# Performance work log

Measured on AMD Instinct MI355X. Metric: run time of the kernel, lower is better.

The kernel has to match this reference:

```python
import jax, jax.numpy as jnp
import numpy as np

N = 50000      # nodes
E = 800000     # edges (before self-loops)
IN = 256       # in_channels
OUT = 64       # out_channels per head
H = 4          # heads (layer 0)
LEAKY = 0.2    # PyG GATConv negative_slope default


def setup_inputs() -> dict:
    key = jax.random.key(0)
    ks = jax.random.split(key, 16)
    g = 0.1
    inp = {
        "x": jax.random.normal(ks[0], (N, IN), jnp.float32),
        "edge_index": jax.random.randint(ks[1], (2, E), 0, N, dtype=jnp.int32),
        # layer 0: in -> H*OUT, concat=True
        "W0": jax.random.normal(ks[2], (IN, H * OUT), jnp.float32) * g,
        "a_src0": jax.random.normal(ks[3], (H, OUT), jnp.float32) * g,
        "a_dst0": jax.random.normal(ks[4], (H, OUT), jnp.float32) * g,
        "b0": jnp.zeros((H * OUT,), jnp.float32),
        # layer 1: H*OUT -> OUT, heads=1, concat=False
        "W1": jax.random.normal(ks[5], (H * OUT, OUT), jnp.float32) * g,
        "a_src1": jax.random.normal(ks[6], (1, OUT), jnp.float32) * g,
        "a_dst1": jax.random.normal(ks[7], (1, OUT), jnp.float32) * g,
        "b1": jnp.zeros((OUT,), jnp.float32),
        # layer 2: H*OUT -> OUT (input is OUT from layer 1? no: layer1 outputs OUT)
        "W2": jax.random.normal(ks[8], (OUT, OUT), jnp.float32) * g,
        "a_src2": jax.random.normal(ks[9], (1, OUT), jnp.float32) * g,
        "a_dst2": jax.random.normal(ks[10], (1, OUT), jnp.float32) * g,
        "b2": jnp.zeros((OUT,), jnp.float32),
    }
    return inp


def _gat_layer(x, src, dst, W, a_s, a_d, b, heads, concat):
    """PyG GATConv: per-head linear, edge attention logits, segment softmax
    over incoming edges of each destination node, scatter-sum aggregate."""
    n = x.shape[0]
    h = (x @ W).reshape(n, heads, -1)                      # [N, H, C]
    al_s = (h * a_s).sum(-1)                               # [N, H]
    al_d = (h * a_d).sum(-1)                               # [N, H]
    e = jax.nn.leaky_relu(al_s[src] + al_d[dst], LEAKY)    # [E', H]
    m = jax.ops.segment_max(e, dst, num_segments=n)        # [N, H]
    ex = jnp.exp(e - m[dst])
    den = jax.ops.segment_sum(ex, dst, num_segments=n)     # [N, H]
    alpha = ex / (den[dst] + 1e-16)                        # [E', H]
    out = jax.ops.segment_sum(alpha[:, :, None] * h[src], dst, num_segments=n)  # [N,H,C]
    out = out.reshape(n, -1) if concat else out.mean(axis=1)
    return out + b


def reference(x, edge_index, W0, a_src0, a_dst0, b0, W1, a_src1, a_dst1, b1,
              W2, a_src2, a_dst2, b2):
    n = x.shape[0]
    loop = jnp.arange(n, dtype=edge_index.dtype)
    src = jnp.concatenate([edge_index[0], loop])   # PyG add_self_loops=True
    dst = jnp.concatenate([edge_index[1], loop])
    h = _gat_layer(x, src, dst, W0, a_src0, a_dst0, b0, H, True)
    h = jax.nn.elu(h)
    h = _gat_layer(h, src, dst, W1, a_src1, a_dst1, b1, 1, False)
    h = jax.nn.elu(h)
    h = _gat_layer(h, src, dst, W2, a_src2, a_dst2, b2, 1, False)
    h = jax.nn.elu(h)
    return h
```

## Files before the change

### kernel.cpp

```cpp
#include <hip/hip_runtime.h>
#include <hip/hip_bf16.h>


typedef unsigned short ushort_t;
typedef __attribute__((ext_vector_type(8))) short short8;
typedef __attribute__((ext_vector_type(4))) float f32x4;

__device__ __forceinline__ float elu_f(float x){ return x > 0.f ? x : expm1f(x); }
__device__ __forceinline__ float lrelu_f(float x){ return x > 0.f ? x : 0.2f * x; }
__device__ __forceinline__ ushort_t f2b(float f){
  union { float f; unsigned u; } v; v.f = f;
  unsigned r = v.u + 0x7fff + ((v.u >> 16) & 1);
  return (ushort_t)(r >> 16);
}
__device__ __forceinline__ float b2f_lo(unsigned v){
  union { unsigned u; float f; } c; c.u = v << 16; return c.f;
}
__device__ __forceinline__ float b2f_hi(unsigned v){
  union { unsigned u; float f; } c; c.u = v & 0xffff0000u; return c.f;
}

__global__ __launch_bounds__(256) void prep_kernel(const int* __restrict__ ei,
                                                   int* __restrict__ cnt,
                                                   const float4* __restrict__ x4,
                                                   ushort4* __restrict__ xb4, int n4,
                                                   const float* __restrict__ W0,
                                                   ushort_t* __restrict__ W0p,
                                                   const float* __restrict__ W1,
                                                   ushort_t* __restrict__ W1p,
                                                   const float* __restrict__ W2,
                                                   ushort_t* __restrict__ W2p,
                                                   int E, int Etot, int eb, int fb){
  int bid = blockIdx.x; int t = threadIdx.x;
  if(bid < eb){
    int e = bid * 256 + t;
    if(e < Etot){
      int d = (e < E) ? ei[E + e] : (e - E);
      atomicAdd(&cnt[d], 1);
    }
  } else if(bid < eb + fb){
    int i = (bid - eb) * 256 + t;
    if(i < n4){
      float4 v = x4[i];
      ushort4 o;
      o.x = f2b(v.x); o.y = f2b(v.y); o.z = f2b(v.z); o.w = f2b(v.w);
      xb4[i] = o;
    }
  } else {
    int r = bid - eb - fb;
    if(r < 256){
      int i = r * 256 + t; int k = i >> 8, n = i & 255;
      W0p[(size_t)n * 256 + k] = f2b(W0[i]);
    } else if(r < 320){
      int i = (r - 256) * 256 + t; int k = i >> 6, n = i & 63;
      W1p[(size_t)n * 256 + k] = f2b(W1[i]);
    } else {
      int i = (r - 320) * 256 + t; int k = i >> 6, n = i & 63;
      W2p[(size_t)n * 64 + k] = f2b(W2[i]);
    }
  }
}

__global__ __launch_bounds__(256) void blocksum_kernel(const int* __restrict__ cnt,
                                                       int* __restrict__ bsum, int N){
  __shared__ int sm[256];
  int t = threadIdx.x;
  int i = blockIdx.x * 256 + t;
  sm[t] = (i < N) ? cnt[i] : 0;
  __syncthreads();
  for(int off = 128; off > 0; off >>= 1){
    if(t < off) sm[t] += sm[t + off];
    __syncthreads();
  }
  if(t == 0) bsum[blockIdx.x] = sm[0];
}

__global__ __launch_bounds__(256) void scan2_kernel(const int* __restrict__ cnt,
                                                    const int* __restrict__ bsum,
                                                    int* __restrict__ rowptr,
                                                    int* __restrict__ cursor,
                                                    int N, int Etot, int nb){
  __shared__ int sm[256];
  __shared__ int spfx;
  int t = threadIdx.x;
  int c = blockIdx.x;
  sm[t] = (t < c && t < nb) ? bsum[t] : 0;
  __syncthreads();
  for(int off = 128; off > 0; off >>= 1){
    if(t < off) sm[t] += sm[t + off];
    __syncthreads();
  }
  if(t == 0) spfx = sm[0];
  __syncthreads();
  int pfx = spfx;
  __syncthreads();
  int i = c * 256 + t;
  int v = (i < N) ? cnt[i] : 0;
  sm[t] = v;
  __syncthreads();
  for(int off = 1; off < 256; off <<= 1){
    int x = 0;
    if(t >= off) x = sm[t - off];
    __syncthreads();
    sm[t] += x;
    __syncthreads();
  }
  if(i < N){
    int ex = sm[t] - v + pfx;
    rowptr[i] = ex;
    cursor[i] = ex;
    if(i == N - 1) rowptr[N] = Etot;
  }
}

__global__ __launch_bounds__(256) void scatter_kernel(const int* __restrict__ ei,
                                                      int* __restrict__ cursor,
                                                      int* __restrict__ esrc,
                                                      int E, int Etot){
  int e = blockIdx.x * 256 + threadIdx.x;
  if(e >= Etot) return;
  int s, d;
  if(e < E){ s = ei[e]; d = ei[E + e]; } else { s = e - E; d = s; }
  int pos = atomicAdd(&cursor[d], 1);
  esrc[pos] = s;
}

#define SKP 264
__global__ __launch_bounds__(256) void gemm0_kernel(const ushort_t* __restrict__ A,
                                                    const ushort_t* __restrict__ Bp,
                                                    ushort_t* __restrict__ h0b,
                                                    const float* __restrict__ asrc,
                                                    const float* __restrict__ adst,
                                                    float* __restrict__ als,
                                                    float* __restrict__ ald, int M){
  __shared__ ushort_t As[32 * SKP];
  int t = threadIdx.x;
  int row0 = blockIdx.x * 32;
  {
    int c = t;
    #pragma unroll
    for(int it = 0; it < 4; it++, c += 256){
      int r = c >> 5;
      int kc = (c & 31) << 3;
      int gr = row0 + r;
      short8 v = {};
      if(gr < M) v = *(const short8*)(A + (size_t)gr * 256 + kc);
      *(short8*)(As + r * SKP + kc) = v;
    }
  }
  __syncthreads();
  int wave = t >> 6, lane = t & 63;
  int m = lane & 15, q = lane >> 4;
  int colb = wave;
  const ushort_t* Bq = Bp + (size_t)(colb * 64 + m) * 256 + q * 8;
  const ushort_t* A0 = As + m * SKP + q * 8;
  const ushort_t* A1 = As + (16 + m) * SKP + q * 8;
  f32x4 acc[2][4] = {};
  for(int k0 = 0; k0 < 256; k0 += 32){
    short8 bv[4];
    #pragma unroll
    for(int j = 0; j < 4; j++) bv[j] = *(const short8*)(Bq + (size_t)j * 16 * 256 + k0);
    short8 a0 = *(const short8*)(A0 + k0);
    short8 a1 = *(const short8*)(A1 + k0);
    #pragma unroll
    for(int j = 0; j < 4; j++){
      acc[0][j] = __builtin_amdgcn_mfma_f32_16x16x32_bf16(a0, bv[j], acc[0][j], 0, 0, 0);
      acc[1][j] = __builtin_amdgcn_mfma_f32_16x16x32_bf16(a1, bv[j], acc[1][j], 0, 0, 0);
    }
  }
  #pragma unroll
  for(int rt = 0; rt < 2; rt++){
    #pragma unroll
    for(int j = 0; j < 4; j++){
      int col = colb * 64 + j * 16 + m;
      #pragma unroll
      for(int i = 0; i < 4; i++){
        int gr = row0 + rt * 16 + q * 4 + i;
        if(gr < M) h0b[(size_t)gr * 256 + col] = f2b(acc[rt][j][i]);
      }
    }
    float vs[4] = {0,0,0,0}, vd[4] = {0,0,0,0};
    #pragma unroll
    for(int j = 0; j < 4; j++){
      int col = colb * 64 + j * 16 + m;
      float a_s = asrc[col], a_d = adst[col];
      #pragma unroll
      for(int i = 0; i < 4; i++){
        vs[i] = fmaf(acc[rt][j][i], a_s, vs[i]);
        vd[i] = fmaf(acc[rt][j][i], a_d, vd[i]);
      }
    }
    #pragma unroll
    for(int off = 8; off > 0; off >>= 1){
      #pragma unroll
      for(int i = 0; i < 4; i++){
        vs[i] += __shfl_down(vs[i], off, 16);
        vd[i] += __shfl_down(vd[i], off, 16);
      }
    }
    if(m == 0){
      #pragma unroll
      for(int i = 0; i < 4; i++){
        int gr = row0 + rt * 16 + q * 4 + i;
        if(gr < M){
          als[(size_t)gr * 4 + colb] = vs[i];
          ald[(size_t)gr * 4 + colb] = vd[i];
        }
      }
    }
  }
}

#define SKP2 264
__global__ __launch_bounds__(256, 8) void agg0g1_kernel(const int* __restrict__ rowptr,
                                                        const int* __restrict__ esrc,
                                                        const uint2* __restrict__ h0b2,
                                                        const float4* __restrict__ als4,
                                                        const float4* __restrict__ ald4,
                                                        const float4* __restrict__ b4,
                                                        const ushort_t* __restrict__ W1p,
                                                        const float* __restrict__ as1,
                                                        const float* __restrict__ ad1,
                                                        ushort_t* __restrict__ g1b,
                                                        float* __restrict__ als1,
                                                        float* __restrict__ ald1, int N){
  __shared__ ushort_t Hs[16 * SKP2];
  __shared__ float aps[4][16], apd[4][16];
  int t = threadIdx.x;
  int lane = t & 63;
  int wave = t >> 6;
  int nbase = blockIdx.x * 16;
  int h = lane >> 4;
  float4 bb = b4[lane];
  for(int j = 0; j < 4; j++){
    int n = nbase + wave * 4 + j;
    int nl = wave * 4 + j;
    uint2 o; o.x = 0u; o.y = 0u;
    if(n < N){
      int beg = rowptr[n], end = rowptr[n + 1];
      float adh = ((const float*)(ald4 + n))[h];
      float4 acc = make_float4(0.f, 0.f, 0.f, 0.f);
      float den = 0.f;
      for(int c0 = beg; c0 < end; c0 += 16){
        int e = c0 + (lane & 15);
        int s = n; float w = 0.f;
        if(e < end){
          s = esrc[e];
          w = expf(lrelu_f(((const float*)(als4 + s))[h] + adh));
        }
        int rem = end - c0;
        if(rem > 16) rem = 16;
        #pragma unroll
        for(int g = 0; g < 4; g++){
          if(g * 4 < rem){
            int si[4]; float wi[4]; uint2 v[4];
            #pragma unroll
            for(int ii = 0; ii < 4; ii++){
              int idx = (lane & 48) + g * 4 + ii;
              si[ii] = __shfl(s, idx, 64);
              wi[ii] = __shfl(w, idx, 64);
            }
            #pragma unroll
            for(int ii = 0; ii < 4; ii++)
              v[ii] = h0b2[((size_t)si[ii] << 6) + lane];
            #pragma unroll
            for(int ii = 0; ii < 4; ii++){
              acc.x = fmaf(wi[ii], b2f_lo(v[ii].x), acc.x);
              acc.y = fmaf(wi[ii], b2f_hi(v[ii].x), acc.y);
              acc.z = fmaf(wi[ii], b2f_lo(v[ii].y), acc.z);
              acc.w = fmaf(wi[ii], b2f_hi(v[ii].y), acc.w);
              den += wi[ii];
            }
          }
        }
      }
      float inv = 1.f / (den + 1e-16f);
      float v0 = elu_f(acc.x * inv + bb.x);
      float v1 = elu_f(acc.y * inv + bb.y);
      float v2 = elu_f(acc.z * inv + bb.z);
      float v3 = elu_f(acc.w * inv + bb.w);
      o.x = (unsigned)f2b(v0) | ((unsigned)f2b(v1) << 16);
      o.y = (unsigned)f2b(v2) | ((unsigned)f2b(v3) << 16);
    }
    *(uint2*)(Hs + nl * SKP2 + lane * 4) = o;
  }
  __syncthreads();
  int m = lane & 15, q = lane >> 4;
  const ushort_t* Bw = W1p + (size_t)(wave * 16 + m) * 256 + q * 8;
  const ushort_t* Aw = Hs + m * SKP2 + q * 8;
  f32x4 acc1 = {};
  #pragma unroll
  for(int k0 = 0; k0 < 256; k0 += 32){
    short8 av = *(const short8*)(Aw + k0);
    short8 bv = *(const short8*)(Bw + k0);
    acc1 = __builtin_amdgcn_mfma_f32_16x16x32_bf16(av, bv, acc1, 0, 0, 0);
  }
  #pragma unroll
  for(int i = 0; i < 4; i++){
    int gn = nbase + q * 4 + i;
    if(gn < N) g1b[(size_t)gn * 64 + wave * 16 + m] = f2b(acc1[i]);
  }
  float a_s = as1[wave * 16 + m], a_d = ad1[wave * 16 + m];
  float vs[4], vd[4];
  #pragma unroll
  for(int i = 0; i < 4; i++){
    vs[i] = acc1[i] * a_s;
    vd[i] = acc1[i] * a_d;
  }
  #pragma unroll
  for(int off = 8; off > 0; off >>= 1){
    #pragma unroll
    for(int i = 0; i < 4; i++){
      vs[i] += __shfl_down(vs[i], off, 16);
      vd[i] += __shfl_down(vd[i], off, 16);
    }
  }
  if(m == 0){
    #pragma unroll
    for(int i = 0; i < 4; i++){
      aps[wave][q * 4 + i] = vs[i];
      apd[wave][q * 4 + i] = vd[i];
    }
  }
  __syncthreads();
  if(t < 16){
    int gn = nbase + t;
    if(gn < N){
      als1[gn] = aps[0][t] + aps[1][t] + aps[2][t] + aps[3][t];
      ald1[gn] = apd[0][t] + apd[1][t] + apd[2][t] + apd[3][t];
    }
  }
}

#define H2S 72
__global__ __launch_bounds__(256, 8) void agg1g2_kernel(const int* __restrict__ rowptr,
                                                        const int* __restrict__ esrc,
                                                        const uint2* __restrict__ g1b2,
                                                        const float* __restrict__ als1,
                                                        const float* __restrict__ ald1,
                                                        const float* __restrict__ b1,
                                                        const ushort_t* __restrict__ W2p,
                                                        const float* __restrict__ as2,
                                                        const float* __restrict__ ad2,
                                                        ushort_t* __restrict__ g2b,
                                                        float* __restrict__ als2,
                                                        float* __restrict__ ald2, int N){
  __shared__ ushort_t Hs[16 * H2S];
  __shared__ float aps[4][16], apd[4][16];
  int t = threadIdx.x;
  int wave = t >> 6, lane = t & 63;
  int nbase = blockIdx.x * 16;
  int g = lane >> 4;
  int p = lane & 15;
  int n = nbase + wave * 4 + g;
  int nl = wave * 4 + g;
  if(n < N){
    int beg = rowptr[n], end = rowptr[n + 1];
    float ad = ald1[n];
    float4 acc = make_float4(0.f, 0.f, 0.f, 0.f);
    float den = 0.f;
    for(int c0 = beg; c0 < end; c0 += 16){
      int e = c0 + p;
      int s = n; float w = 0.f;
      if(e < end){
        s = esrc[e];
        w = expf(lrelu_f(als1[s] + ad));
      }
      int rem = end - c0;
      if(rem > 16) rem = 16;
      #pragma unroll
      for(int gg = 0; gg < 4; gg++){
        if(gg * 4 < rem){
          #pragma unroll
          for(int ii = 0; ii < 4; ii++){
            int i = gg * 4 + ii;
            int idx = (lane & 48) + i;
            int si = __shfl(s, idx, 64);
            float wi = __shfl(w, idx, 64);
            uint2 v = g1b2[((size_t)si << 4) + p];
            acc.x = fmaf(wi, b2f_lo(v.x), acc.x);
            acc.y = fmaf(wi, b2f_hi(v.x), acc.y);
            acc.z = fmaf(wi, b2f_lo(v.y), acc.z);
            acc.w = fmaf(wi, b2f_hi(v.y), acc.w);
            den += wi;
          }
        }
      }
    }
    float inv = 1.f / (den + 1e-16f);
    float4 bb = ((const float4*)b1)[p];
    unsigned o0 = (unsigned)f2b(elu_f(acc.x * inv + bb.x)) |
                  ((unsigned)f2b(elu_f(acc.y * inv + bb.y)) << 16);
    unsigned o1 = (unsigned)f2b(elu_f(acc.z * inv + bb.z)) |
                  ((unsigned)f2b(elu_f(acc.w * inv + bb.w)) << 16);
    uint2 ov; ov.x = o0; ov.y = o1;
    *(uint2*)(Hs + nl * H2S + p * 4) = ov;
  }
  __syncthreads();
  int m = lane & 15, q = lane >> 4;
  const ushort_t* Bw = W2p + (size_t)(wave * 16 + m) * 64 + q * 8;
  const ushort_t* Aw = Hs + m * H2S + q * 8;
  f32x4 acc = {};
  #pragma unroll
  for(int k0 = 0; k0 < 64; k0 += 32){
    short8 av = *(const short8*)(Aw + k0);
    short8 bv = *(const short8*)(Bw + k0);
    acc = __builtin_amdgcn_mfma_f32_16x16x32_bf16(av, bv, acc, 0, 0, 0);
  }
  float a_s = as2[wave * 16 + m], a_d = ad2[wave * 16 + m];
  float vs[4], vd[4];
  #pragma unroll
  for(int i = 0; i < 4; i++){
    int gn = nbase + q * 4 + i;
    if(gn < N) g2b[(size_t)gn * 64 + wave * 16 + m] = f2b(acc[i]);
    vs[i] = acc[i] * a_s;
    vd[i] = acc[i] * a_d;
  }
  #pragma unroll
  for(int off = 8; off > 0; off >>= 1){
    #pragma unroll
    for(int i = 0; i < 4; i++){
      vs[i] += __shfl_down(vs[i], off, 16);
      vd[i] += __shfl_down(vd[i], off, 16);
    }
  }
  if(m == 0){
    #pragma unroll
    for(int i = 0; i < 4; i++){
      aps[wave][q * 4 + i] = vs[i];
      apd[wave][q * 4 + i] = vd[i];
    }
  }
  __syncthreads();
  if(t < 16){
    int gn = nbase + t;
    if(gn < N){
      als2[gn] = aps[0][t] + aps[1][t] + aps[2][t] + aps[3][t];
      ald2[gn] = apd[0][t] + apd[1][t] + apd[2][t] + apd[3][t];
    }
  }
}

__global__ __launch_bounds__(256, 8) void aggF_kernel(const int* __restrict__ rowptr,
                                                      const int* __restrict__ esrc,
                                                      const uint2* __restrict__ gb2,
                                                      const float* __restrict__ als,
                                                      const float* __restrict__ ald,
                                                      const float* __restrict__ b,
                                                      float4* __restrict__ outp, int N){
  int t = threadIdx.x;
  int lane = t & 63;
  int g = lane >> 4;
  int p = lane & 15;
  int n = blockIdx.x * 16 + (t >> 6) * 4 + g;
  if(n >= N) return;
  int beg = rowptr[n], end = rowptr[n + 1];
  float ad = ald[n];
  float4 acc = make_float4(0.f, 0.f, 0.f, 0.f);
  float den = 0.f;
  for(int c0 = beg; c0 < end; c0 += 16){
    int e = c0 + p;
    int s = n; float w = 0.f;
    if(e < end){
      s = esrc[e];
      w = expf(lrelu_f(als[s] + ad));
    }
    int rem = end - c0;
    if(rem > 16) rem = 16;
    #pragma unroll
    for(int gg = 0; gg < 4; gg++){
      if(gg * 4 < rem){
        #pragma unroll
        for(int ii = 0; ii < 4; ii++){
          int i = gg * 4 + ii;
          int idx = (lane & 48) + i;
          int si = __shfl(s, idx, 64);
          float wi = __shfl(w, idx, 64);
          uint2 v = gb2[((size_t)si << 4) + p];
          acc.x = fmaf(wi, b2f_lo(v.x), acc.x);
          acc.y = fmaf(wi, b2f_hi(v.x), acc.y);
          acc.z = fmaf(wi, b2f_lo(v.y), acc.z);
          acc.w = fmaf(wi, b2f_hi(v.y), acc.w);
          den += wi;
        }
      }
    }
  }
  float inv = 1.f / (den + 1e-16f);
  float4 bb = ((const float4*)b)[p];
  float4 o;
  o.x = elu_f(acc.x * inv + bb.x);
  o.y = elu_f(acc.y * inv + bb.y);
  o.z = elu_f(acc.z * inv + bb.z);
  o.w = elu_f(acc.w * inv + bb.w);
  outp[((size_t)n << 4) + p] = o;
}

extern "C" void kernel_launch(void* const* d_in, const int* in_sizes, int n_in,
                              void* d_out, int out_size, void* d_ws, size_t ws_size,
                              hipStream_t stream){
  const float* x   = (const float*)d_in[0];
  const int*   ei  = (const int*)d_in[1];
  const float* W0  = (const float*)d_in[2];
  const float* as0 = (const float*)d_in[3];
  const float* ad0 = (const float*)d_in[4];
  const float* b0  = (const float*)d_in[5];
  const float* W1  = (const float*)d_in[6];
  const float* as1 = (const float*)d_in[7];
  const float* ad1 = (const float*)d_in[8];
  const float* b1  = (const float*)d_in[9];
  const float* W2  = (const float*)d_in[10];
  const float* as2 = (const float*)d_in[11];
  const float* ad2 = (const float*)d_in[12];
  const float* b2  = (const float*)d_in[13];
  int N = in_sizes[0] / 256;
  int E = in_sizes[1] / 2;
  int Etot = E + N;

  size_t off = 0;
  auto alc = [&](size_t bytes) -> char* {
    char* p = (char*)d_ws + off;
    off += (bytes + 255) & ~(size_t)255;
    return p;
  };
  ushort_t* xb    = (ushort_t*)alc((size_t)N * 256 * 2);
  ushort_t* h0b   = (ushort_t*)alc((size_t)N * 256 * 2);
  float*    als   = (float*)alc((size_t)N * 4 * 4);
  float*    ald   = (float*)alc((size_t)N * 4 * 4);
  float*    als1  = (float*)alc((size_t)N * 4);
  float*    ald1  = (float*)alc((size_t)N * 4);
  float*    als2  = (float*)alc((size_t)N * 4);
  float*    ald2  = (float*)alc((size_t)N * 4);
  int*      esrc  = (int*)alc((size_t)Etot * 4);
  int*      rowptr= (int*)alc((size_t)(N + 1) * 4);
  int*      cnt   = (int*)alc((size_t)N * 4);
  int*      cursor= (int*)alc((size_t)N * 4);
  int*      bsum  = (int*)alc(256 * 4);
  ushort_t* W0p   = (ushort_t*)alc(256 * 256 * 2);
  ushort_t* W1p   = (ushort_t*)alc(256 * 64 * 2);
  ushort_t* W2p   = (ushort_t*)alc(64 * 64 * 2);

  ushort_t* g1b = xb;
  ushort_t* g2b = h0b;

  int nb = (N + 255) / 256;
  int eb = (Etot + 255) / 256;
  int fb = (N * 64 + 255) / 256;
  int g0b = (N + 31) / 32;
  int tb = (N + 15) / 16;
  int ab16 = (N + 15) / 16;

  hipMemsetAsync(cnt, 0, (size_t)N * 4, stream);
  prep_kernel<<<eb + fb + 336, 256, 0, stream>>>(ei, cnt, (const float4*)x,
                                                 (ushort4*)xb, N * 64,
                                                 W0, W0p, W1, W1p, W2, W2p,
                                                 E, Etot, eb, fb);
  blocksum_kernel<<<nb, 256, 0, stream>>>(cnt, bsum, N);
  scan2_kernel<<<nb, 256, 0, stream>>>(cnt, bsum, rowptr, cursor, N, Etot, nb);
  scatter_kernel<<<eb, 256, 0, stream>>>(ei, cursor, esrc, E, Etot);

  gemm0_kernel<<<g0b, 256, 0, stream>>>(xb, W0p, h0b, as0, ad0, als, ald, N);

  agg0g1_kernel<<<ab16, 256, 0, stream>>>(rowptr, esrc, (const uint2*)h0b,
                                          (const float4*)als, (const float4*)ald,
                                          (const float4*)b0, W1p, as1, ad1,
                                          g1b, als1, ald1, N);

  agg1g2_kernel<<<tb, 256, 0, stream>>>(rowptr, esrc, (const uint2*)g1b,
                                        als1, ald1, b1, W2p, as2, ad2,
                                        g2b, als2, ald2, N);

  aggF_kernel<<<ab16, 256, 0, stream>>>(rowptr, esrc, (const uint2*)g2b,
                                        als2, ald2, b2, (float4*)d_out, N);
}
```

Measured before the change: 360.0 us.

## Fuse x bf16 conversion into gemm0 load and double agg0g1 node tile

The separate pass that converted x to bf16 in prep_kernel is removed. gemm0 now reads fp32 x directly and converts it to bf16 while filling shared memory, which saves one full write and read of a 25MB intermediate. agg0g1 now handles 32 nodes per block instead of 16, running two MFMA row tiles per wave so each block's W1 loads are reused across more nodes. The larger shared-memory tile and longer per-wave loop may lower occupancy and leave fewer blocks for load balancing.

```diff
diff --git a/kernel.cpp b/kernel.cpp
--- a/kernel.cpp
+++ b/kernel.cpp
@@ -22,15 +22,13 @@
 
 __global__ __launch_bounds__(256) void prep_kernel(const int* __restrict__ ei,
                                                    int* __restrict__ cnt,
-                                                   const float4* __restrict__ x4,
-                                                   ushort4* __restrict__ xb4, int n4,
                                                    const float* __restrict__ W0,
                                                    ushort_t* __restrict__ W0p,
                                                    const float* __restrict__ W1,
                                                    ushort_t* __restrict__ W1p,
                                                    const float* __restrict__ W2,
                                                    ushort_t* __restrict__ W2p,
-                                                   int E, int Etot, int eb, int fb){
+                                                   int E, int Etot, int eb){
   int bid = blockIdx.x; int t = threadIdx.x;
   if(bid < eb){
     int e = bid * 256 + t;
@@ -38,16 +36,8 @@
       int d = (e < E) ? ei[E + e] : (e - E);
       atomicAdd(&cnt[d], 1);
     }
-  } else if(bid < eb + fb){
-    int i = (bid - eb) * 256 + t;
-    if(i < n4){
-      float4 v = x4[i];
-      ushort4 o;
-      o.x = f2b(v.x); o.y = f2b(v.y); o.z = f2b(v.z); o.w = f2b(v.w);
-      xb4[i] = o;
-    }
   } else {
-    int r = bid - eb - fb;
+    int r = bid - eb;
     if(r < 256){
       int i = r * 256 + t; int k = i >> 8, n = i & 255;
       W0p[(size_t)n * 256 + k] = f2b(W0[i]);
@@ -126,7 +116,7 @@
 }
 
 #define SKP 264
-__global__ __launch_bounds__(256) void gemm0_kernel(const ushort_t* __restrict__ A,
+__global__ __launch_bounds__(256) void gemm0_kernel(const float4* __restrict__ x4,
                                                     const ushort_t* __restrict__ Bp,
                                                     ushort_t* __restrict__ h0b,
                                                     const float* __restrict__ asrc,
@@ -144,7 +134,14 @@
       int kc = (c & 31) << 3;
       int gr = row0 + r;
       short8 v = {};
-      if(gr < M) v = *(const short8*)(A + (size_t)gr * 256 + kc);
+      if(gr < M){
+        float4 f0 = x4[(size_t)gr * 64 + (kc >> 2)];
+        float4 f1 = x4[(size_t)gr * 64 + (kc >> 2) + 1];
+        v[0] = (short)f2b(f0.x); v[1] = (short)f2b(f0.y);
+        v[2] = (short)f2b(f0.z); v[3] = (short)f2b(f0.w);
+        v[4] = (short)f2b(f1.x); v[5] = (short)f2b(f1.y);
+        v[6] = (short)f2b(f1.z); v[7] = (short)f2b(f1.w);
+      }
       *(short8*)(As + r * SKP + kc) = v;
     }
   }
@@ -224,17 +221,17 @@
                                                         ushort_t* __restrict__ g1b,
                                                         float* __restrict__ als1,
                                                         float* __restrict__ ald1, int N){
-  __shared__ ushort_t Hs[16 * SKP2];
-  __shared__ float aps[4][16], apd[4][16];
+  __shared__ ushort_t Hs[32 * SKP2];
+  __shared__ float aps[4][32], apd[4][32];
   int t = threadIdx.x;
   int lane = t & 63;
   int wave = t >> 6;
-  int nbase = blockIdx.x * 16;
+  int nbase = blockIdx.x * 32;
   int h = lane >> 4;
   float4 bb = b4[lane];
-  for(int j = 0; j < 4; j++){
-    int n = nbase + wave * 4 + j;
-    int nl = wave * 4 + j;
+  for(int j = 0; j < 8; j++){
+    int n = nbase + wave * 8 + j;
+    int nl = wave * 8 + j;
     uint2 o; o.x = 0u; o.y = 0u;
     if(n < N){
       int beg = rowptr[n], end = rowptr[n + 1];
@@ -287,43 +284,46 @@
   __syncthreads();
   int m = lane & 15, q = lane >> 4;
   const ushort_t* Bw = W1p + (size_t)(wave * 16 + m) * 256 + q * 8;
-  const ushort_t* Aw = Hs + m * SKP2 + q * 8;
-  f32x4 acc1 = {};
+  float a_s = as1[wave * 16 + m], a_d = ad1[wave * 16 + m];
   #pragma unroll
-  for(int k0 = 0; k0 < 256; k0 += 32){
-    short8 av = *(const short8*)(Aw + k0);
-    short8 bv = *(const short8*)(Bw + k0);
-    acc1 = __builtin_amdgcn_mfma_f32_16x16x32_bf16(av, bv, acc1, 0, 0, 0);
-  }
-  #pragma unroll
-  for(int i = 0; i < 4; i++){
-    int gn = nbase + q * 4 + i;
-    if(gn < N) g1b[(size_t)gn * 64 + wave * 16 + m] = f2b(acc1[i]);
-  }
-  float a_s = as1[wave * 16 + m], a_d = ad1[wave * 16 + m];
-  float vs[4], vd[4];
-  #pragma unroll
-  for(int i = 0; i < 4; i++){
-    vs[i] = acc1[i] * a_s;
-    vd[i] = acc1[i] * a_d;
-  }
-  #pragma unroll
-  for(int off = 8; off > 0; off >>= 1){
+  for(int rt = 0; rt < 2; rt++){
+    const ushort_t* Aw = Hs + (rt * 16 + m) * SKP2 + q * 8;
+    f32x4 acc1 = {};
+    #pragma unroll
+    for(int k0 = 0; k0 < 256; k0 += 32){
+      short8 av = *(const short8*)(Aw + k0);
+      short8 bv = *(const short8*)(Bw + k0);
+      acc1 = __builtin_amdgcn_mfma_f32_16x16x32_bf16(av, bv, acc1, 0, 0, 0);
+    }
     #pragma unroll
     for(int i = 0; i < 4; i++){
-      vs[i] += __shfl_down(vs[i], off, 16);
-      vd[i] += __shfl_down(vd[i], off, 16);
-    }
-  }
-  if(m == 0){
+      int gn = nbase + rt * 16 + q * 4 + i;
+      if(gn < N) g1b[(size_t)gn * 64 + wave * 16 + m] = f2b(acc1[i]);
+    }
+    float vs[4], vd[4];
     #pragma unroll
     for(int i = 0; i < 4; i++){
-      aps[wave][q * 4 + i] = vs[i];
-      apd[wave][q * 4 + i] = vd[i];
-    }
-  }
-  __syncthreads();
-  if(t < 16){
+      vs[i] = acc1[i] * a_s;
+      vd[i] = acc1[i] * a_d;
+    }
+    #pragma unroll
+    for(int off = 8; off > 0; off >>= 1){
+      #pragma unroll
+      for(int i = 0; i < 4; i++){
+        vs[i] += __shfl_down(vs[i], off, 16);
+        vd[i] += __shfl_down(vd[i], off, 16);
+      }
+    }
+    if(m == 0){
+      #pragma unroll
+      for(int i = 0; i < 4; i++){
+        aps[wave][rt * 16 + q * 4 + i] = vs[i];
+        apd[wave][rt * 16 + q * 4 + i] = vd[i];
+      }
+    }
+  }
+  __syncthreads();
+  if(t < 32){
     int gn = nbase + t;
     if(gn < N){
       als1[gn] = aps[0][t] + aps[1][t] + aps[2][t] + aps[3][t];
@@ -523,7 +523,7 @@
     off += (bytes + 255) & ~(size_t)255;
     return p;
   };
-  ushort_t* xb    = (ushort_t*)alc((size_t)N * 256 * 2);
+  ushort_t* g1b   = (ushort_t*)alc((size_t)N * 64 * 2);
   ushort_t* h0b   = (ushort_t*)alc((size_t)N * 256 * 2);
   float*    als   = (float*)alc((size_t)N * 4 * 4);
   float*    ald   = (float*)alc((size_t)N * 4 * 4);
@@ -540,28 +540,26 @@
   ushort_t* W1p   = (ushort_t*)alc(256 * 64 * 2);
   ushort_t* W2p   = (ushort_t*)alc(64 * 64 * 2);
 
-  ushort_t* g1b = xb;
   ushort_t* g2b = h0b;
 
   int nb = (N + 255) / 256;
   int eb = (Etot + 255) / 256;
-  int fb = (N * 64 + 255) / 256;
   int g0b = (N + 31) / 32;
   int tb = (N + 15) / 16;
+  int ab32 = (N + 31) / 32;
   int ab16 = (N + 15) / 16;
 
   hipMemsetAsync(cnt, 0, (size_t)N * 4, stream);
-  prep_kernel<<<eb + fb + 336, 256, 0, stream>>>(ei, cnt, (const float4*)x,
-                                                 (ushort4*)xb, N * 64,
-                                                 W0, W0p, W1, W1p, W2, W2p,
-                                                 E, Etot, eb, fb);
+  prep_kernel<<<eb + 336, 256, 0, stream>>>(ei, cnt, W0, W0p, W1, W1p, W2, W2p,
+                                            E, Etot, eb);
   blocksum_kernel<<<nb, 256, 0, stream>>>(cnt, bsum, N);
   scan2_kernel<<<nb, 256, 0, stream>>>(cnt, bsum, rowptr, cursor, N, Etot, nb);
   scatter_kernel<<<eb, 256, 0, stream>>>(ei, cursor, esrc, E, Etot);
 
-  gemm0_kernel<<<g0b, 256, 0, stream>>>(xb, W0p, h0b, as0, ad0, als, ald, N);
-
-  agg0g1_kernel<<<ab16, 256, 0, stream>>>(rowptr, esrc, (const uint2*)h0b,
+  gemm0_kernel<<<g0b, 256, 0, stream>>>((const float4*)x, W0p, h0b,
+                                        as0, ad0, als, ald, N);
+
+  agg0g1_kernel<<<ab32, 256, 0, stream>>>(rowptr, esrc, (const uint2*)h0b,
                                           (const float4*)als, (const float4*)ald,
                                           (const float4*)b0, W1p, as1, ad1,
                                           g1b, als1, ald1, N);
```

Result: no change. 359.7 us (-0.1%).
